# Kernel optimization log

Measured on AMD Instinct MI355X. Metric: run time of the kernel, lower is better.

## Reference

```python
import jax, jax.numpy as jnp
import numpy as np

NUM_CLASSES = 6     # terrain classes 0..5
NUM_SUBJECTS = 16   # subject ids 0..15
MARGIN = 1.0
EPS = 1e-6          # torch pairwise_distance eps (added to the difference)


def setup_inputs() -> dict:
    key = jax.random.key(0)
    k1, k2, k3 = jax.random.split(key, 3)
    B, D = 131072, 256
    emb = jax.random.normal(k1, (B, D), dtype=jnp.float32)
    labels = jax.random.randint(k2, (B,), 0, NUM_CLASSES)
    sbj = jax.random.randint(k3, (B,), 0, NUM_SUBJECTS)
    return {"emb": emb, "labels": labels, "sbj": sbj}


def reference(emb, labels, sbj):
    """Within-subject hard-negative triplet loss.

    For every (subject s, class c) group with >=2 positives and >=1 negative
    (negatives = same subject, different class):
      anchor = first positive (in batch order), positive = second positive,
      negative = hardest (closest to anchor) same-subject other-class sample.
    Loss = mean over valid triplets of relu(d(a,p) - d(a,n) + margin), p=2.
    """
    B, D = emb.shape
    # flat grid of all (subject, class) pairs: P = NUM_SUBJECTS * NUM_CLASSES
    s_grid = jnp.repeat(jnp.arange(NUM_SUBJECTS), NUM_CLASSES)
    c_grid = jnp.tile(jnp.arange(NUM_CLASSES), NUM_SUBJECTS)

    def per_pair(s, c):
        m_pos = (sbj == s) & (labels == c)          # (B,)
        m_neg = (sbj == s) & (labels != c)          # (B,)
        cs = jnp.cumsum(m_pos)
        anchor_idx = jnp.argmax(m_pos & (cs == 1))  # first positive in batch order
        pos_idx = jnp.argmax(m_pos & (cs == 2))     # second positive
        valid = (jnp.sum(m_pos) >= 2) & (jnp.sum(m_neg) >= 1)
        return anchor_idx, pos_idx, m_neg, valid

    anchor_idx, pos_idx, m_neg, valid = jax.vmap(per_pair)(s_grid, c_grid)

    a = emb[anchor_idx]                              # (P, D)
    # squared L2 distance from each anchor to every sample (for mining only;
    # argmin of squared distance == argmin of distance, matching torch.cdist)
    d2 = (jnp.sum(a * a, axis=-1)[:, None]
          + jnp.sum(emb * emb, axis=-1)[None, :]
          - 2.0 * (a @ emb.T))                       # (P, B)
    d2 = jnp.where(m_neg, d2, jnp.inf)
    neg_idx = jnp.argmin(d2, axis=1)                 # (P,) hardest negative

    p = emb[pos_idx]                                 # (P, D)
    n = emb[neg_idx]                                 # (P, D)
    # torch TripletMarginLoss uses pairwise_distance: ||x1 - x2 + eps||_2
    d_ap = jnp.linalg.norm(a - p + EPS, axis=-1)
    d_an = jnp.linalg.norm(a - n + EPS, axis=-1)
    per_triplet = jnp.maximum(d_ap - d_an + MARGIN, 0.0)

    vf = valid.astype(emb.dtype)
    cnt = jnp.sum(vf)
    loss = jnp.sum(per_triplet * vf) / jnp.maximum(cnt, 1.0)
    return jnp.where(cnt > 0, loss, jnp.zeros((), emb.dtype))
```

## Files before the change

kernel.cpp:

```cpp
#include <hip/hip_runtime.h>
#include <hip/hip_bf16.h>

#define NUM_CLASSES 6
#define NUM_SUBJECTS 16
#define NUM_PAIRS (NUM_CLASSES * NUM_SUBJECTS)
#define MARGIN 1.0f
#define EPS 1e-6f
#define INF_I 0x7fffffff

typedef float f32x4 __attribute__((ext_vector_type(4)));
typedef short s16x8 __attribute__((ext_vector_type(8)));


__device__ __forceinline__ unsigned int fkey(float f) {
    unsigned int b = __float_as_uint(f);
    return (b & 0x80000000u) ? ~b : (b | 0x80000000u);
}

__device__ __forceinline__ unsigned int pkbf(float x, float y) {
    unsigned short a = __builtin_bit_cast(unsigned short, __float2bfloat16(x));
    unsigned short b = __builtin_bit_cast(unsigned short, __float2bfloat16(y));
    return (unsigned int)a | ((unsigned int)b << 16);
}

__global__ void k_init(int* min1, int* min2, int* cntPos, int* cntSbj,
                       unsigned long long* best) {
    int t = threadIdx.x;
    if (t < NUM_PAIRS) {
        min1[t] = INF_I;
        min2[t] = INF_I;
        cntPos[t] = 0;
        best[t] = ~0ull;
    }
    if (t < NUM_SUBJECTS) cntSbj[t] = 0;
}

__global__ __launch_bounds__(1024) void k_stats(const int* __restrict__ labels,
                                                const int* __restrict__ sbj,
                                                int* min1, int* min2, int* cntPos,
                                                int* cntSbj, int B) {
    __shared__ int l1[NUM_PAIRS], l2[NUM_PAIRS], lcp[NUM_PAIRS], lcs[NUM_SUBJECTS];
    for (int t = threadIdx.x; t < NUM_PAIRS; t += blockDim.x) { l1[t] = INF_I; l2[t] = INF_I; lcp[t] = 0; }
    if (threadIdx.x < NUM_SUBJECTS) lcs[threadIdx.x] = 0;
    __syncthreads();
    for (int i = blockIdx.x * blockDim.x + threadIdx.x; i < B; i += gridDim.x * blockDim.x) {
        int s = sbj[i], c = labels[i];
        int p = s * NUM_CLASSES + c;
        int o = atomicMin(&l1[p], i);
        atomicMin(&l2[p], max(o, i));
        atomicAdd(&lcp[p], 1);
        atomicAdd(&lcs[s], 1);
    }
    __syncthreads();
    for (int t = threadIdx.x; t < NUM_PAIRS; t += blockDim.x) {
        int m1 = l1[t];
        if (m1 != INF_I) {
            int o = atomicMin(&min1[t], m1);
            atomicMin(&min2[t], max(o, m1));
            if (l2[t] != INF_I) atomicMin(&min2[t], l2[t]);
            atomicAdd(&cntPos[t], lcp[t]);
        }
    }
    if (threadIdx.x < NUM_SUBJECTS && lcs[threadIdx.x]) atomicAdd(&cntSbj[threadIdx.x], lcs[threadIdx.x]);
}

__global__ void k_gather(const float4* __restrict__ emb4, const int* __restrict__ min1,
                         unsigned long long* ancT, int B) {
    int pr = blockIdx.x;
    int l = threadIdx.x;
    int idx = min1[pr];
    if (idx < 0 || idx >= B) idx = 0;
    float4 v = emb4[(size_t)idx * 64 + l];
    unsigned long long u = (unsigned long long)pkbf(v.x, v.y)
                         | ((unsigned long long)pkbf(v.z, v.w) << 32);
    ancT[pr * 64 + l] = u;
}

__global__ __launch_bounds__(512, 6) void k_mine(const float4* __restrict__ emb4,
                                                 const int* __restrict__ labels,
                                                 const int* __restrict__ sbj,
                                                 const unsigned long long* __restrict__ ancT,
                                                 unsigned long long* gbest, int B) {
    __shared__ __align__(16) char ldsA[64 * 512];
    __shared__ __align__(16) char ldsB[96 * 128];
    __shared__ float e2s[64];
    __shared__ int sbjT[64], lblT[64];
    __shared__ unsigned long long lbest[NUM_PAIRS];

    const int t = threadIdx.x;
    const int R0 = (int)blockIdx.x * 64;
    const int lane = t & 63;
    const int wv = t >> 6;

    for (int u = t; u < NUM_PAIRS; u += blockDim.x) lbest[u] = ~0ull;

#pragma unroll
    for (int it = 0; it < 8; ++it) {
        int fi = it * 512 + t;
        float4 v = emb4[(size_t)R0 * 64 + fi];
        int row = it * 8 + wv;
        unsigned long long u = (unsigned long long)pkbf(v.x, v.y)
                             | ((unsigned long long)pkbf(v.z, v.w) << 32);
        int off = (lane * 8) ^ ((row & 7) << 4);
        *(unsigned long long*)(ldsA + row * 512 + off) = u;
    }
    if (t < 64) { sbjT[t] = sbj[R0 + t]; lblT[t] = labels[R0 + t]; }

    const int rt = wv & 3;
    const int ch = wv >> 2;
    const int col = lane & 15;
    const int rloc = rt * 16 + col;
    const int asw = (col & 7) << 4;
    const int kgrp = (lane >> 4) << 4;

    f32x4 acc[3];
#pragma unroll
    for (int ct = 0; ct < 3; ++ct) acc[ct] = f32x4{0.f, 0.f, 0.f, 0.f};
    f32x4 aG = f32x4{0.f, 0.f, 0.f, 0.f};

#pragma unroll
    for (int kq = 0; kq < 4; ++kq) {
        if (kq > 0) __syncthreads();
        {
            const ulonglong2* src = (const ulonglong2*)ancT;
            int u = t;
            if (u < 768) {
                int pair = u >> 3, w = u & 7;
                ulonglong2 val = src[pair * 32 + kq * 8 + w];
                *(ulonglong2*)(ldsB + pair * 128 + ((w * 16) ^ ((pair & 7) << 4))) = val;
            }
            u = t + 512;
            if (u < 768) {
                int pair = u >> 3, w = u & 7;
                ulonglong2 val = src[pair * 32 + kq * 8 + w];
                *(ulonglong2*)(ldsB + pair * 128 + ((w * 16) ^ ((pair & 7) << 4))) = val;
            }
        }
        __syncthreads();
#pragma unroll
        for (int ksl = 0; ksl < 2; ++ksl) {
            int kbB = ksl * 64 + kgrp;
            int kbA = kq * 128 + kbB;
            s16x8 a = *(const s16x8*)(ldsA + rloc * 512 + (kbA ^ asw));
            if (ch == 0)
                aG = __builtin_amdgcn_mfma_f32_16x16x32_bf16(a, a, aG, 0, 0, 0);
#pragma unroll
            for (int ct = 0; ct < 3; ++ct) {
                int p = (ch * 3 + ct) * 16 + col;
                s16x8 b = *(const s16x8*)(ldsB + p * 128 + (kbB ^ ((p & 7) << 4)));
                acc[ct] = __builtin_amdgcn_mfma_f32_16x16x32_bf16(a, b, acc[ct], 0, 0, 0);
            }
        }
    }
    if (ch == 0 && (lane >> 4) == (col >> 2)) e2s[rt * 16 + col] = aG[col & 3];
    __syncthreads();

    const int rb = rt * 16 + ((lane >> 4) << 2);
    float e2r[4]; int sr[4], lr[4];
#pragma unroll
    for (int r = 0; r < 4; ++r) { e2r[r] = e2s[rb + r]; sr[r] = sbjT[rb + r]; lr[r] = lblT[rb + r]; }
#pragma unroll
    for (int ct = 0; ct < 3; ++ct) {
        int p = (ch * 3 + ct) * 16 + col;
        int sp = p / NUM_CLASSES, cp = p - sp * NUM_CLASSES;
#pragma unroll
        for (int r = 0; r < 4; ++r) {
            if (sr[r] == sp && lr[r] != cp) {
                float key = e2r[r] - 2.0f * acc[ct][r];
                unsigned long long pk =
                    ((unsigned long long)fkey(key) << 32) | (unsigned int)(R0 + rb + r);
                atomicMin(&lbest[p], pk);
            }
        }
    }
    __syncthreads();
    for (int u = t; u < NUM_PAIRS; u += blockDim.x) {
        unsigned long long v = lbest[u];
        if (v != ~0ull) {
            unsigned long long cur = gbest[u];
            if (v < cur) atomicMin(&gbest[u], v);
        }
    }
}

__global__ __launch_bounds__(1024) void k_finalize(const float4* __restrict__ emb4,
                                                   const int* __restrict__ min1,
                                                   const int* __restrict__ min2,
                                                   const int* __restrict__ cntPos,
                                                   const int* __restrict__ cntSbj,
                                                   const unsigned long long* __restrict__ best,
                                                   float* out, int B) {
    __shared__ float vals[NUM_PAIRS];
    __shared__ int vld[NUM_PAIRS];
    int wave = threadIdx.x >> 6;
    int lane = threadIdx.x & 63;
    for (int p = wave; p < NUM_PAIRS; p += (blockDim.x >> 6)) {
        int s = p / NUM_CLASSES;
        int ai = min1[p], pi = min2[p];
        int npos = cntPos[p];
        int nneg = cntSbj[s] - npos;
        unsigned long long bb = best[p];
        int ni = (int)(bb & 0xffffffffu);
        bool ok = (npos >= 2) && (nneg >= 1) && (bb != ~0ull);
        if (ai < 0 || ai >= B) ai = 0;
        if (pi < 0 || pi >= B) pi = 0;
        if (ni < 0 || ni >= B) ni = 0;
        float4 a = emb4[(size_t)ai * 64 + lane];
        float4 pp = emb4[(size_t)pi * 64 + lane];
        float4 nn = emb4[(size_t)ni * 64 + lane];
        float dap = 0.f, dan = 0.f, tt;
        tt = a.x - pp.x + EPS; dap += tt * tt;
        tt = a.y - pp.y + EPS; dap += tt * tt;
        tt = a.z - pp.z + EPS; dap += tt * tt;
        tt = a.w - pp.w + EPS; dap += tt * tt;
        tt = a.x - nn.x + EPS; dan += tt * tt;
        tt = a.y - nn.y + EPS; dan += tt * tt;
        tt = a.z - nn.z + EPS; dan += tt * tt;
        tt = a.w - nn.w + EPS; dan += tt * tt;
#pragma unroll
        for (int m = 32; m >= 1; m >>= 1) {
            dap += __shfl_xor(dap, m, 64);
            dan += __shfl_xor(dan, m, 64);
        }
        if (lane == 0) {
            float lv = sqrtf(dap) - sqrtf(dan) + MARGIN;
            vals[p] = ok ? fmaxf(lv, 0.f) : 0.f;
            vld[p] = ok ? 1 : 0;
        }
    }
    __syncthreads();
    if (threadIdx.x == 0) {
        float sum = 0.f;
        int cnt = 0;
        for (int p = 0; p < NUM_PAIRS; ++p) { sum += vals[p]; cnt += vld[p]; }
        out[0] = (cnt > 0) ? (sum / (float)cnt) : 0.f;
    }
}

extern "C" void kernel_launch(void* const* d_in, const int* in_sizes, int n_in,
                              void* d_out, int out_size, void* d_ws, size_t ws_size,
                              hipStream_t stream) {
    const float* emb = (const float*)d_in[0];
    const int* labels = (const int*)d_in[1];
    const int* sbj = (const int*)d_in[2];
    float* out = (float*)d_out;
    const int B = in_sizes[1];
    const float4* emb4 = (const float4*)emb;

    char* ws = (char*)d_ws;
    int* min1 = (int*)(ws + 0);
    int* min2 = (int*)(ws + 384);
    int* cntPos = (int*)(ws + 768);
    int* cntSbj = (int*)(ws + 1152);
    unsigned long long* best = (unsigned long long*)(ws + 1216);
    unsigned long long* ancT = (unsigned long long*)(ws + 2048);

    k_init<<<1, 128, 0, stream>>>(min1, min2, cntPos, cntSbj, best);

    k_stats<<<128, 1024, 0, stream>>>(labels, sbj, min1, min2, cntPos, cntSbj, B);

    k_gather<<<NUM_PAIRS, 64, 0, stream>>>(emb4, min1, ancT, B);

    k_mine<<<B / 64, 512, 0, stream>>>(emb4, labels, sbj, ancT, best, B);

    k_finalize<<<1, 1024, 0, stream>>>(emb4, min1, min2, cntPos, cntSbj, best, out, B);
}
```

Measured before the change: 65.18 us.

## Process two row tiles per block with register prefetch of the second tile

Each mining block now handles two 64-row tiles instead of one, halving the grid size. The second tile's embeddings are loaded into registers while the first tile's MFMA work runs, then packed into LDS afterward. The per-block shared-best reduction and the global atomic flush are amortized over twice as many rows. In exchange, the anchor tile is reloaded into LDS for each tile, register pressure rises from the prefetch buffer, and the grid has fewer blocks to spread across CUs.

```diff
diff --git a/kernel.cpp b/kernel.cpp
--- a/kernel.cpp
+++ b/kernel.cpp
@@ -88,23 +88,10 @@
     __shared__ unsigned long long lbest[NUM_PAIRS];
 
     const int t = threadIdx.x;
-    const int R0 = (int)blockIdx.x * 64;
     const int lane = t & 63;
     const int wv = t >> 6;
 
     for (int u = t; u < NUM_PAIRS; u += blockDim.x) lbest[u] = ~0ull;
-
-#pragma unroll
-    for (int it = 0; it < 8; ++it) {
-        int fi = it * 512 + t;
-        float4 v = emb4[(size_t)R0 * 64 + fi];
-        int row = it * 8 + wv;
-        unsigned long long u = (unsigned long long)pkbf(v.x, v.y)
-                             | ((unsigned long long)pkbf(v.z, v.w) << 32);
-        int off = (lane * 8) ^ ((row & 7) << 4);
-        *(unsigned long long*)(ldsA + row * 512 + off) = u;
-    }
-    if (t < 64) { sbjT[t] = sbj[R0 + t]; lblT[t] = labels[R0 + t]; }
 
     const int rt = wv & 3;
     const int ch = wv >> 2;
@@ -112,65 +99,110 @@
     const int rloc = rt * 16 + col;
     const int asw = (col & 7) << 4;
     const int kgrp = (lane >> 4) << 4;
-
-    f32x4 acc[3];
-#pragma unroll
-    for (int ct = 0; ct < 3; ++ct) acc[ct] = f32x4{0.f, 0.f, 0.f, 0.f};
-    f32x4 aG = f32x4{0.f, 0.f, 0.f, 0.f};
-
-#pragma unroll
-    for (int kq = 0; kq < 4; ++kq) {
-        if (kq > 0) __syncthreads();
+    const int arow = wv;
+    const int aoff = (lane * 8);
+
+    const int tile0 = (int)blockIdx.x * 2;
+
+    {
+        int R0 = tile0 * 64;
+#pragma unroll
+        for (int it = 0; it < 8; ++it) {
+            float4 v = emb4[(size_t)R0 * 64 + it * 512 + t];
+            int row = it * 8 + arow;
+            unsigned long long u = (unsigned long long)pkbf(v.x, v.y)
+                                 | ((unsigned long long)pkbf(v.z, v.w) << 32);
+            *(unsigned long long*)(ldsA + row * 512 + (aoff ^ ((row & 7) << 4))) = u;
+        }
+        if (t < 64) { sbjT[t] = sbj[R0 + t]; lblT[t] = labels[R0 + t]; }
+    }
+
+    float4 pf[8];
+
+#pragma unroll
+    for (int ti = 0; ti < 2; ++ti) {
+        const int R0 = (tile0 + ti) * 64;
+        if (ti == 0) {
+            int R1 = (tile0 + 1) * 64;
+#pragma unroll
+            for (int it = 0; it < 8; ++it)
+                pf[it] = emb4[(size_t)R1 * 64 + it * 512 + t];
+        }
+
+        f32x4 acc[3];
+#pragma unroll
+        for (int ct = 0; ct < 3; ++ct) acc[ct] = f32x4{0.f, 0.f, 0.f, 0.f};
+        f32x4 aG = f32x4{0.f, 0.f, 0.f, 0.f};
+
+#pragma unroll
+        for (int kq = 0; kq < 4; ++kq) {
+            __syncthreads();
+            {
+                const ulonglong2* src = (const ulonglong2*)ancT;
+                int u = t;
+                if (u < 768) {
+                    int pair = u >> 3, w = u & 7;
+                    ulonglong2 val = src[pair * 32 + kq * 8 + w];
+                    *(ulonglong2*)(ldsB + pair * 128 + ((w * 16) ^ ((pair & 7) << 4))) = val;
+                }
+                u = t + 512;
+                if (u < 768) {
+                    int pair = u >> 3, w = u & 7;
+                    ulonglong2 val = src[pair * 32 + kq * 8 + w];
+                    *(ulonglong2*)(ldsB + pair * 128 + ((w * 16) ^ ((pair & 7) << 4))) = val;
+                }
+            }
+            __syncthreads();
+#pragma unroll
+            for (int ksl = 0; ksl < 2; ++ksl) {
+                int kbB = ksl * 64 + kgrp;
+                int kbA = kq * 128 + kbB;
+                s16x8 a = *(const s16x8*)(ldsA + rloc * 512 + (kbA ^ asw));
+                if (ch == 0)
+                    aG = __builtin_amdgcn_mfma_f32_16x16x32_bf16(a, a, aG, 0, 0, 0);
+#pragma unroll
+                for (int ct = 0; ct < 3; ++ct) {
+                    int p = (ch * 3 + ct) * 16 + col;
+                    s16x8 b = *(const s16x8*)(ldsB + p * 128 + (kbB ^ ((p & 7) << 4)));
+                    acc[ct] = __builtin_amdgcn_mfma_f32_16x16x32_bf16(a, b, acc[ct], 0, 0, 0);
+                }
+            }
+        }
+        if (ch == 0 && (lane >> 4) == (col >> 2)) e2s[rt * 16 + col] = aG[col & 3];
+        __syncthreads();
+
         {
-            const ulonglong2* src = (const ulonglong2*)ancT;
-            int u = t;
-            if (u < 768) {
-                int pair = u >> 3, w = u & 7;
-                ulonglong2 val = src[pair * 32 + kq * 8 + w];
-                *(ulonglong2*)(ldsB + pair * 128 + ((w * 16) ^ ((pair & 7) << 4))) = val;
-            }
-            u = t + 512;
-            if (u < 768) {
-                int pair = u >> 3, w = u & 7;
-                ulonglong2 val = src[pair * 32 + kq * 8 + w];
-                *(ulonglong2*)(ldsB + pair * 128 + ((w * 16) ^ ((pair & 7) << 4))) = val;
-            }
-        }
-        __syncthreads();
-#pragma unroll
-        for (int ksl = 0; ksl < 2; ++ksl) {
-            int kbB = ksl * 64 + kgrp;
-            int kbA = kq * 128 + kbB;
-            s16x8 a = *(const s16x8*)(ldsA + rloc * 512 + (kbA ^ asw));
-            if (ch == 0)
-                aG = __builtin_amdgcn_mfma_f32_16x16x32_bf16(a, a, aG, 0, 0, 0);
+            const int rb = rt * 16 + ((lane >> 4) << 2);
+            float e2r[4]; int sr[4], lr[4];
+#pragma unroll
+            for (int r = 0; r < 4; ++r) { e2r[r] = e2s[rb + r]; sr[r] = sbjT[rb + r]; lr[r] = lblT[rb + r]; }
 #pragma unroll
             for (int ct = 0; ct < 3; ++ct) {
                 int p = (ch * 3 + ct) * 16 + col;
-                s16x8 b = *(const s16x8*)(ldsB + p * 128 + (kbB ^ ((p & 7) << 4)));
-                acc[ct] = __builtin_amdgcn_mfma_f32_16x16x32_bf16(a, b, acc[ct], 0, 0, 0);
-            }
-        }
-    }
-    if (ch == 0 && (lane >> 4) == (col >> 2)) e2s[rt * 16 + col] = aG[col & 3];
-    __syncthreads();
-
-    const int rb = rt * 16 + ((lane >> 4) << 2);
-    float e2r[4]; int sr[4], lr[4];
-#pragma unroll
-    for (int r = 0; r < 4; ++r) { e2r[r] = e2s[rb + r]; sr[r] = sbjT[rb + r]; lr[r] = lblT[rb + r]; }
-#pragma unroll
-    for (int ct = 0; ct < 3; ++ct) {
-        int p = (ch * 3 + ct) * 16 + col;
-        int sp = p / NUM_CLASSES, cp = p - sp * NUM_CLASSES;
-#pragma unroll
-        for (int r = 0; r < 4; ++r) {
-            if (sr[r] == sp && lr[r] != cp) {
-                float key = e2r[r] - 2.0f * acc[ct][r];
-                unsigned long long pk =
-                    ((unsigned long long)fkey(key) << 32) | (unsigned int)(R0 + rb + r);
-                atomicMin(&lbest[p], pk);
-            }
+                int sp = p / NUM_CLASSES, cp = p - sp * NUM_CLASSES;
+#pragma unroll
+                for (int r = 0; r < 4; ++r) {
+                    if (sr[r] == sp && lr[r] != cp) {
+                        float key = e2r[r] - 2.0f * acc[ct][r];
+                        unsigned long long pk =
+                            ((unsigned long long)fkey(key) << 32) | (unsigned int)(R0 + rb + r);
+                        atomicMin(&lbest[p], pk);
+                    }
+                }
+            }
+        }
+
+        if (ti == 0) {
+            __syncthreads();
+#pragma unroll
+            for (int it = 0; it < 8; ++it) {
+                int row = it * 8 + arow;
+                unsigned long long u = (unsigned long long)pkbf(pf[it].x, pf[it].y)
+                                     | ((unsigned long long)pkbf(pf[it].z, pf[it].w) << 32);
+                *(unsigned long long*)(ldsA + row * 512 + (aoff ^ ((row & 7) << 4))) = u;
+            }
+            int R1 = (tile0 + 1) * 64;
+            if (t < 64) { sbjT[t] = sbj[R1 + t]; lblT[t] = labels[R1 + t]; }
         }
     }
     __syncthreads();
@@ -261,7 +293,7 @@
 
     k_gather<<<NUM_PAIRS, 64, 0, stream>>>(emb4, min1, ancT, B);
 
-    k_mine<<<B / 64, 512, 0, stream>>>(emb4, labels, sbj, ancT, best, B);
+    k_mine<<<B / 128, 512, 0, stream>>>(emb4, labels, sbj, ancT, best, B);
 
     k_finalize<<<1, 1024, 0, stream>>>(emb4, min1, min2, cntPos, cntSbj, best, out, B);
 }
```

After: 85.02 us. 1.3x slower.
